# Performance work log

Measured on AMD Instinct MI355X. Metric: run time of the kernel, lower is better.

## Reference

```python
import jax, jax.numpy as jnp
import numpy as np

# pywt Wavelet('db4') decomposition filters (dec_lo, dec_hi), 8 taps
DEC_LO = jnp.array([-0.010597401784997278, 0.032883011666982945, 0.030841381835986965,
                    -0.18703481171888114, -0.02798376941698385, 0.6308807679295904,
                    0.7148465705525415, 0.23037781330885523], dtype=jnp.float32)
DEC_HI = jnp.array([-0.23037781330885523, 0.7148465705525415, -0.6308807679295904,
                    -0.02798376941698385, 0.18703481171888114, 0.030841381835986965,
                    -0.032883011666982945, -0.010597401784997278], dtype=jnp.float32)
FILT_LEN = 8
LEVEL = 3


def _dwt_step(a):
    """Single-level DWT matching pywt.dwt(a, 'db4', mode='symmetric') along last axis.

    pywt equivalence: np.convolve(np.pad(x, L-1, 'symmetric'), f, 'valid')[1::2].
    np.convolve flips the filter, so we cross-correlate with the reversed filter,
    starting at offset 1 with stride 2.
    a: [B, N] -> (cA, cD) each [B, floor((N + L - 1)/2)]
    """
    p = FILT_LEN - 1
    xp = jnp.pad(a, ((0, 0), (p, p)), mode='symmetric')[:, 1:]  # [B, N+2p-1]
    k = jnp.stack([DEC_LO[::-1], DEC_HI[::-1]])[:, None, :]      # [2, 1, L] (OIH)
    y = jax.lax.conv_general_dilated(
        xp[:, None, :].astype(a.dtype), k.astype(a.dtype),
        window_strides=(2,), padding='VALID',
        dimension_numbers=('NCH', 'OIH', 'NCH'))                 # [B, 2, M]
    return y[:, 0, :], y[:, 1, :]


def wavedec_features(x):
    """pywt.wavedec(x, 'db4', level=3) -> concat of flattened [cA3, cD3, cD2, cD1]."""
    a = x
    details = []
    for _ in range(LEVEL):
        a, d = _dwt_step(a)
        details.append(d)
    coeffs = [a] + details[::-1]
    return jnp.concatenate([c.reshape(-1) for c in coeffs])


def setup_inputs() -> dict:
    key = jax.random.key(0)
    x = jax.random.normal(key, (4096, 8192), dtype=jnp.float32)
    return {"x": x}


def reference(x):
    return wavedec_features(x)
```

## Files before the change

### kernel.cpp

```cpp
#include <hip/hip_runtime.h>


constexpr int N0 = 8192;
constexpr int M1 = 4099;
constexpr int M2 = 2053;
constexpr int M3 = 1030;
constexpr int NT = 256;

constexpr int C1 = 1023;
constexpr int C2 = 511;
constexpr int C3 = 255;

__device__ __forceinline__ int symidx(int o, int n) {
    if (o < 0) o = -1 - o;
    if (o >= n) o = 2 * n - 1 - o;
    return o;
}

__device__ __forceinline__ void compute4(const float* __restrict__ w,
                                         float* __restrict__ a,
                                         float* __restrict__ d) {
    constexpr float RLO[8] = {0.23037781330885523f,  0.7148465705525415f,
                              0.6308807679295904f,   -0.02798376941698385f,
                              -0.18703481171888114f, 0.030841381835986965f,
                              0.032883011666982945f, -0.010597401784997278f};
    constexpr float RHI[8] = {-0.010597401784997278f, -0.032883011666982945f,
                              0.030841381835986965f,  0.18703481171888114f,
                              -0.02798376941698385f,  -0.6308807679295904f,
                              0.7148465705525415f,    -0.23037781330885523f};
#pragma unroll
    for (int j = 0; j < 4; ++j) {
        float aj = 0.f, dj = 0.f;
#pragma unroll
        for (int t = 0; t < 8; ++t) {
            const float v = w[2 * j + 2 + t];
            aj = fmaf(RLO[t], v, aj);
            dj = fmaf(RHI[t], v, dj);
        }
        a[j] = aj;
        d[j] = dj;
    }
}

__device__ __forceinline__ void edge_pair(const float* in, int n, int i,
                                          float& a, float& d) {
    constexpr float LO[8] = {
        -0.010597401784997278f, 0.032883011666982945f, 0.030841381835986965f,
        -0.18703481171888114f,  -0.02798376941698385f, 0.6308807679295904f,
        0.7148465705525415f,    0.23037781330885523f};
    constexpr float HI[8] = {
        -0.23037781330885523f,  0.7148465705525415f,   -0.6308807679295904f,
        -0.02798376941698385f,  0.18703481171888114f,  0.030841381835986965f,
        -0.032883011666982945f, -0.010597401784997278f};
    a = 0.f;
    d = 0.f;
#pragma unroll
    for (int s = 0; s < 8; ++s) {
        const float v = in[symidx(2 * i + 1 - s, n)];
        a = fmaf(LO[s], v, a);
        d = fmaf(HI[s], v, d);
    }
}

__global__ __launch_bounds__(NT) void WaveletFeatures_77214922047612_kernel(
    const float* __restrict__ x, float* __restrict__ out, int B) {
    __shared__ __align__(16) float s1[M1 + 1];
    __shared__ __align__(16) float s2[M2 + 3];

    const int row = blockIdx.x;
    const int tid = threadIdx.x;
    const float* xr = x + (size_t)row * N0;

    float* ca3 = out + (size_t)row * M3;
    float* cd3 = out + (size_t)B * M3 + (size_t)row * M3;
    float* cd2 = out + 2 * (size_t)B * M3 + (size_t)row * M2;
    float* cd1 = out + (size_t)B * (2 * M3 + M2) + (size_t)row * M1;

    for (int c = tid; c < C1; c += NT) {
        const int i0 = 4 + 4 * c;
        float w[16];
        const float4* p = reinterpret_cast<const float4*>(xr + 2 * i0 - 8);
        *reinterpret_cast<float4*>(&w[0]) = p[0];
        *reinterpret_cast<float4*>(&w[4]) = p[1];
        *reinterpret_cast<float4*>(&w[8]) = p[2];
        *reinterpret_cast<float4*>(&w[12]) = p[3];
        float a[4], d[4];
        compute4(w, a, d);
        *reinterpret_cast<float4*>(&s1[i0]) = make_float4(a[0], a[1], a[2], a[3]);
        cd1[i0 + 0] = d[0];
        cd1[i0 + 1] = d[1];
        cd1[i0 + 2] = d[2];
        cd1[i0 + 3] = d[3];
    }
    if (tid < 7) {
        const int i = tid < 4 ? tid : 4092 + tid;
        float a, d;
        edge_pair(xr, N0, i, a, d);
        s1[i] = a;
        cd1[i] = d;
    }
    __syncthreads();

    for (int c = tid; c < C2; c += NT) {
        const int i0 = 4 + 4 * c;
        float w[16];
        const float4* p = reinterpret_cast<const float4*>(&s1[2 * i0 - 8]);
        *reinterpret_cast<float4*>(&w[0]) = p[0];
        *reinterpret_cast<float4*>(&w[4]) = p[1];
        *reinterpret_cast<float4*>(&w[8]) = p[2];
        *reinterpret_cast<float4*>(&w[12]) = p[3];
        float a[4], d[4];
        compute4(w, a, d);
        *reinterpret_cast<float4*>(&s2[i0]) = make_float4(a[0], a[1], a[2], a[3]);
        cd2[i0 + 0] = d[0];
        cd2[i0 + 1] = d[1];
        cd2[i0 + 2] = d[2];
        cd2[i0 + 3] = d[3];
    }
    if (tid < 9) {
        const int i = tid < 4 ? tid : 2044 + tid;
        float a, d;
        edge_pair(s1, M1, i, a, d);
        s2[i] = a;
        cd2[i] = d;
    }
    __syncthreads();

    for (int c = tid; c < C3; c += NT) {
        const int i0 = 4 + 4 * c;
        float w[16];
        const float4* p = reinterpret_cast<const float4*>(&s2[2 * i0 - 8]);
        *reinterpret_cast<float4*>(&w[0]) = p[0];
        *reinterpret_cast<float4*>(&w[4]) = p[1];
        *reinterpret_cast<float4*>(&w[8]) = p[2];
        *reinterpret_cast<float4*>(&w[12]) = p[3];
        float a[4], d[4];
        compute4(w, a, d);
#pragma unroll
        for (int j = 0; j < 4; ++j) {
            ca3[i0 + j] = a[j];
            cd3[i0 + j] = d[j];
        }
    }
    if (tid < 10) {
        const int i = tid < 4 ? tid : 1020 + tid;
        float a, d;
        edge_pair(s2, M2, i, a, d);
        ca3[i] = a;
        cd3[i] = d;
    }
}

extern "C" void kernel_launch(void* const* d_in, const int* in_sizes, int n_in,
                              void* d_out, int out_size, void* d_ws,
                              size_t ws_size, hipStream_t stream) {
    const float* x = (const float*)d_in[0];
    float* out = (float*)d_out;
    const int B = in_sizes[0] / N0;
    WaveletFeatures_77214922047612_kernel<<<dim3(B), dim3(NT), 0, stream>>>(
        x, out, B);
}
```

Before: 47.49 us.

## Use 512 threads with 8-output level-1 chunks and nontemporal stores

Doubles the block to 512 threads so each pass runs as a single iteration. Level-1 threads now compute 8 outputs from a 24-float window, cutting overlapping halo loads, and the edge handling is extended to match. All global coefficient stores become nontemporal to avoid cache pollution. The launch-bounds occupancy hint may constrain register allocation.

```diff
diff --git a/kernel.cpp b/kernel.cpp
--- a/kernel.cpp
+++ b/kernel.cpp
@@ -5,9 +5,9 @@
 constexpr int M1 = 4099;
 constexpr int M2 = 2053;
 constexpr int M3 = 1030;
-constexpr int NT = 256;
+constexpr int NT = 512;
 
-constexpr int C1 = 1023;
+constexpr int C1 = 511;
 constexpr int C2 = 511;
 constexpr int C3 = 255;
 
@@ -62,7 +62,7 @@
     }
 }
 
-__global__ __launch_bounds__(NT) void WaveletFeatures_77214922047612_kernel(
+__global__ __launch_bounds__(NT, 8) void WaveletFeatures_77214922047612_kernel(
     const float* __restrict__ x, float* __restrict__ out, int B) {
     __shared__ __align__(16) float s1[M1 + 1];
     __shared__ __align__(16) float s2[M2 + 3];
@@ -76,78 +76,76 @@
     float* cd2 = out + 2 * (size_t)B * M3 + (size_t)row * M2;
     float* cd1 = out + (size_t)B * (2 * M3 + M2) + (size_t)row * M1;
 
-    for (int c = tid; c < C1; c += NT) {
-        const int i0 = 4 + 4 * c;
-        float w[16];
+    if (tid < C1) {
+        const int i0 = 4 + 8 * tid;
+        float w[24];
         const float4* p = reinterpret_cast<const float4*>(xr + 2 * i0 - 8);
-        *reinterpret_cast<float4*>(&w[0]) = p[0];
-        *reinterpret_cast<float4*>(&w[4]) = p[1];
-        *reinterpret_cast<float4*>(&w[8]) = p[2];
-        *reinterpret_cast<float4*>(&w[12]) = p[3];
-        float a[4], d[4];
+#pragma unroll
+        for (int k = 0; k < 6; ++k)
+            *reinterpret_cast<float4*>(&w[4 * k]) = p[k];
+        float a[8], d[8];
         compute4(w, a, d);
+        compute4(w + 8, a + 4, d + 4);
         *reinterpret_cast<float4*>(&s1[i0]) = make_float4(a[0], a[1], a[2], a[3]);
-        cd1[i0 + 0] = d[0];
-        cd1[i0 + 1] = d[1];
-        cd1[i0 + 2] = d[2];
-        cd1[i0 + 3] = d[3];
+        *reinterpret_cast<float4*>(&s1[i0 + 4]) =
+            make_float4(a[4], a[5], a[6], a[7]);
+#pragma unroll
+        for (int j = 0; j < 8; ++j)
+            __builtin_nontemporal_store(d[j], &cd1[i0 + j]);
     }
-    if (tid < 7) {
-        const int i = tid < 4 ? tid : 4092 + tid;
+    if (tid < 11) {
+        const int i = tid < 4 ? tid : 4088 + tid;
         float a, d;
         edge_pair(xr, N0, i, a, d);
         s1[i] = a;
-        cd1[i] = d;
+        __builtin_nontemporal_store(d, &cd1[i]);
     }
     __syncthreads();
 
-    for (int c = tid; c < C2; c += NT) {
-        const int i0 = 4 + 4 * c;
+    if (tid < C2) {
+        const int i0 = 4 + 4 * tid;
         float w[16];
         const float4* p = reinterpret_cast<const float4*>(&s1[2 * i0 - 8]);
-        *reinterpret_cast<float4*>(&w[0]) = p[0];
-        *reinterpret_cast<float4*>(&w[4]) = p[1];
-        *reinterpret_cast<float4*>(&w[8]) = p[2];
-        *reinterpret_cast<float4*>(&w[12]) = p[3];
+#pragma unroll
+        for (int k = 0; k < 4; ++k)
+            *reinterpret_cast<float4*>(&w[4 * k]) = p[k];
         float a[4], d[4];
         compute4(w, a, d);
         *reinterpret_cast<float4*>(&s2[i0]) = make_float4(a[0], a[1], a[2], a[3]);
-        cd2[i0 + 0] = d[0];
-        cd2[i0 + 1] = d[1];
-        cd2[i0 + 2] = d[2];
-        cd2[i0 + 3] = d[3];
+#pragma unroll
+        for (int j = 0; j < 4; ++j)
+            __builtin_nontemporal_store(d[j], &cd2[i0 + j]);
     }
     if (tid < 9) {
         const int i = tid < 4 ? tid : 2044 + tid;
         float a, d;
         edge_pair(s1, M1, i, a, d);
         s2[i] = a;
-        cd2[i] = d;
+        __builtin_nontemporal_store(d, &cd2[i]);
     }
     __syncthreads();
 
-    for (int c = tid; c < C3; c += NT) {
-        const int i0 = 4 + 4 * c;
+    if (tid < C3) {
+        const int i0 = 4 + 4 * tid;
         float w[16];
         const float4* p = reinterpret_cast<const float4*>(&s2[2 * i0 - 8]);
-        *reinterpret_cast<float4*>(&w[0]) = p[0];
-        *reinterpret_cast<float4*>(&w[4]) = p[1];
-        *reinterpret_cast<float4*>(&w[8]) = p[2];
-        *reinterpret_cast<float4*>(&w[12]) = p[3];
+#pragma unroll
+        for (int k = 0; k < 4; ++k)
+            *reinterpret_cast<float4*>(&w[4 * k]) = p[k];
         float a[4], d[4];
         compute4(w, a, d);
 #pragma unroll
         for (int j = 0; j < 4; ++j) {
-            ca3[i0 + j] = a[j];
-            cd3[i0 + j] = d[j];
+            __builtin_nontemporal_store(a[j], &ca3[i0 + j]);
+            __builtin_nontemporal_store(d[j], &cd3[i0 + j]);
         }
     }
     if (tid < 10) {
         const int i = tid < 4 ? tid : 1020 + tid;
         float a, d;
         edge_pair(s2, M2, i, a, d);
-        ca3[i] = a;
-        cd3[i] = d;
+        __builtin_nontemporal_store(a, &ca3[i]);
+        __builtin_nontemporal_store(d, &cd3[i]);
     }
 }
 
```

Result: slower. 73.30 us (+54.4%).

## Split each row into two halo-overlapped segments processed by separate blocks

Applied to the files above, without the earlier changes.

Each row is now handled by two blocks, each computing half of the three DWT levels. Each block recomputes a halo of approximation coefficients at the segment boundary so it needs no cross-block communication. This doubles the grid and halves shared memory per block, aiming for more blocks in flight and better latency hiding on a memory-bound kernel. In exchange it adds redundant edge computation and more complex index bookkeeping, and a boundary indexing error would corrupt the output.

```diff
diff --git a/kernel.cpp b/kernel.cpp
--- a/kernel.cpp
+++ b/kernel.cpp
@@ -6,10 +6,6 @@
 constexpr int M2 = 2053;
 constexpr int M3 = 1030;
 constexpr int NT = 256;
-
-constexpr int C1 = 1023;
-constexpr int C2 = 511;
-constexpr int C3 = 255;
 
 __device__ __forceinline__ int symidx(int o, int n) {
     if (o < 0) o = -1 - o;
@@ -42,6 +38,15 @@
     }
 }
 
+__device__ __forceinline__ void load16(const float* __restrict__ p,
+                                       float* __restrict__ w) {
+    *reinterpret_cast<float4*>(&w[0]) = *reinterpret_cast<const float4*>(p);
+    *reinterpret_cast<float4*>(&w[4]) = *reinterpret_cast<const float4*>(p + 4);
+    *reinterpret_cast<float4*>(&w[8]) = *reinterpret_cast<const float4*>(p + 8);
+    *reinterpret_cast<float4*>(&w[12]) =
+        *reinterpret_cast<const float4*>(p + 12);
+}
+
 __device__ __forceinline__ void edge_pair(const float* in, int n, int i,
                                           float& a, float& d) {
     constexpr float LO[8] = {
@@ -64,10 +69,12 @@
 
 __global__ __launch_bounds__(NT) void WaveletFeatures_77214922047612_kernel(
     const float* __restrict__ x, float* __restrict__ out, int B) {
-    __shared__ __align__(16) float s1[M1 + 1];
-    __shared__ __align__(16) float s2[M2 + 3];
+    __shared__ __align__(16) float s1buf[2068];
+    __shared__ __align__(16) float s2buf[1036];
 
-    const int row = blockIdx.x;
+    const int bid = blockIdx.x;
+    const int row = bid >> 1;
+    const int seg = bid & 1;
     const int tid = threadIdx.x;
     const float* xr = x + (size_t)row * N0;
 
@@ -76,78 +83,100 @@
     float* cd2 = out + 2 * (size_t)B * M3 + (size_t)row * M2;
     float* cd1 = out + (size_t)B * (2 * M3 + M2) + (size_t)row * M1;
 
-    for (int c = tid; c < C1; c += NT) {
-        const int i0 = 4 + 4 * c;
-        float w[16];
-        const float4* p = reinterpret_cast<const float4*>(xr + 2 * i0 - 8);
-        *reinterpret_cast<float4*>(&w[0]) = p[0];
-        *reinterpret_cast<float4*>(&w[4]) = p[1];
-        *reinterpret_cast<float4*>(&w[8]) = p[2];
-        *reinterpret_cast<float4*>(&w[12]) = p[3];
-        float a[4], d[4];
-        compute4(w, a, d);
-        *reinterpret_cast<float4*>(&s1[i0]) = make_float4(a[0], a[1], a[2], a[3]);
-        cd1[i0 + 0] = d[0];
-        cd1[i0 + 1] = d[1];
-        cd1[i0 + 2] = d[2];
-        cd1[i0 + 3] = d[3];
-    }
-    if (tid < 7) {
-        const int i = tid < 4 ? tid : 4092 + tid;
-        float a, d;
-        edge_pair(xr, N0, i, a, d);
-        s1[i] = a;
-        cd1[i] = d;
+    const int lo1 = seg ? 2046 : 0;
+    const int lo2 = seg ? 1026 : 0;
+    float* const s1g = s1buf + (lo1 & 3) - lo1;
+    float* const s2g = s2buf + (lo2 & 3) - lo2;
+
+    {
+        const int allo = seg ? 2052 : 4;
+        const int C = seg ? 511 : 512;
+        for (int c = tid; c < C; c += NT) {
+            const int i0 = allo + 4 * c;
+            float w[16];
+            load16(xr + 2 * i0 - 8, w);
+            float a[4], d[4];
+            compute4(w, a, d);
+            *reinterpret_cast<float4*>(&s1g[i0]) =
+                make_float4(a[0], a[1], a[2], a[3]);
+            cd1[i0] = d[0]; cd1[i0 + 1] = d[1];
+            cd1[i0 + 2] = d[2]; cd1[i0 + 3] = d[3];
+        }
+        const int nl = seg ? 0 : 4;
+        const int nr = seg ? 3 : 0;
+        const int ne = seg ? 6 : 12;
+        const int exlo = seg ? 2046 : 2052;
+        if (tid < nl + nr + ne) {
+            int i;
+            bool both;
+            if (tid < nl) { i = tid; both = true; }
+            else if (tid < nl + nr) { i = 4096 + tid - nl; both = true; }
+            else { i = exlo + tid - nl - nr; both = false; }
+            float a, d;
+            edge_pair(xr, N0, i, a, d);
+            s1g[i] = a;
+            if (both) cd1[i] = d;
+        }
     }
     __syncthreads();
 
-    for (int c = tid; c < C2; c += NT) {
-        const int i0 = 4 + 4 * c;
-        float w[16];
-        const float4* p = reinterpret_cast<const float4*>(&s1[2 * i0 - 8]);
-        *reinterpret_cast<float4*>(&w[0]) = p[0];
-        *reinterpret_cast<float4*>(&w[4]) = p[1];
-        *reinterpret_cast<float4*>(&w[8]) = p[2];
-        *reinterpret_cast<float4*>(&w[12]) = p[3];
-        float a[4], d[4];
-        compute4(w, a, d);
-        *reinterpret_cast<float4*>(&s2[i0]) = make_float4(a[0], a[1], a[2], a[3]);
-        cd2[i0 + 0] = d[0];
-        cd2[i0 + 1] = d[1];
-        cd2[i0 + 2] = d[2];
-        cd2[i0 + 3] = d[3];
-    }
-    if (tid < 9) {
-        const int i = tid < 4 ? tid : 2044 + tid;
-        float a, d;
-        edge_pair(s1, M1, i, a, d);
-        s2[i] = a;
-        cd2[i] = d;
+    {
+        const int allo = seg ? 1028 : 4;
+        const int C = seg ? 255 : 256;
+        for (int c = tid; c < C; c += NT) {
+            const int i0 = allo + 4 * c;
+            float w[16];
+            load16(s1g + 2 * i0 - 8, w);
+            float a[4], d[4];
+            compute4(w, a, d);
+            *reinterpret_cast<float4*>(&s2g[i0]) =
+                make_float4(a[0], a[1], a[2], a[3]);
+            cd2[i0] = d[0]; cd2[i0 + 1] = d[1];
+            cd2[i0 + 2] = d[2]; cd2[i0 + 3] = d[3];
+        }
+        const int nl = seg ? 0 : 4;
+        const int nr = seg ? 5 : 0;
+        const int ne = seg ? 2 : 4;
+        const int exlo = seg ? 1026 : 1028;
+        if (tid < nl + nr + ne) {
+            int i;
+            bool both;
+            if (tid < nl) { i = tid; both = true; }
+            else if (tid < nl + nr) { i = 2048 + tid - nl; both = true; }
+            else { i = exlo + tid - nl - nr; both = false; }
+            float a, d;
+            edge_pair(s1g, M1, i, a, d);
+            s2g[i] = a;
+            if (both) cd2[i] = d;
+        }
     }
     __syncthreads();
 
-    for (int c = tid; c < C3; c += NT) {
-        const int i0 = 4 + 4 * c;
-        float w[16];
-        const float4* p = reinterpret_cast<const float4*>(&s2[2 * i0 - 8]);
-        *reinterpret_cast<float4*>(&w[0]) = p[0];
-        *reinterpret_cast<float4*>(&w[4]) = p[1];
-        *reinterpret_cast<float4*>(&w[8]) = p[2];
-        *reinterpret_cast<float4*>(&w[12]) = p[3];
-        float a[4], d[4];
-        compute4(w, a, d);
+    {
+        const int allo = seg ? 516 : 4;
+        const int C = 127;
+        for (int c = tid; c < C; c += NT) {
+            const int i0 = allo + 4 * c;
+            float w[16];
+            load16(s2g + 2 * i0 - 8, w);
+            float a[4], d[4];
+            compute4(w, a, d);
 #pragma unroll
-        for (int j = 0; j < 4; ++j) {
-            ca3[i0 + j] = a[j];
-            cd3[i0 + j] = d[j];
+            for (int j = 0; j < 4; ++j) {
+                ca3[i0 + j] = a[j];
+                cd3[i0 + j] = d[j];
+            }
         }
-    }
-    if (tid < 10) {
-        const int i = tid < 4 ? tid : 1020 + tid;
-        float a, d;
-        edge_pair(s2, M2, i, a, d);
-        ca3[i] = a;
-        cd3[i] = d;
+        const int nl = seg ? 0 : 4;
+        const int nr = seg ? 6 : 4;
+        const int alhi = seg ? 1024 : 512;
+        if (tid < nl + nr) {
+            const int i = tid < nl ? tid : alhi + tid - nl;
+            float a, d;
+            edge_pair(s2g, M2, i, a, d);
+            ca3[i] = a;
+            cd3[i] = d;
+        }
     }
 }
 
@@ -157,6 +186,6 @@
     const float* x = (const float*)d_in[0];
     float* out = (float*)d_out;
     const int B = in_sizes[0] / N0;
-    WaveletFeatures_77214922047612_kernel<<<dim3(B), dim3(NT), 0, stream>>>(
+    WaveletFeatures_77214922047612_kernel<<<dim3(2 * B), dim3(NT), 0, stream>>>(
         x, out, B);
 }
```

New measurement: 47.33 us, median of 2. No clear change (-0.3%).
